# Kernel tuning notes

Measured on AMD Instinct MI355X. Metric: run time of the kernel, lower is better.

The kernel has to match this reference:

```python
import jax, jax.numpy as jnp
import numpy as np

B, S, D = 1, 4096, 1024
H, KVH, HD = 16, 4, 64  # heads, kv heads, head_dim; GQA groups = H//KVH
EOS_PROB = 0.05


def rotate_half(x):
    h = x.shape[-1] // 2
    return jnp.concatenate([-x[..., h:], x[..., :h]], axis=-1)


def setup_inputs() -> dict:
    key = jax.random.key(0)
    ks = jax.random.split(key, 8)
    hidden_states = jax.random.normal(ks[0], (B, S, D), jnp.float32) * 0.02
    # standard RoPE tables, [B, S, HD]
    inv_freq = 1.0 / (10000.0 ** (jnp.arange(0, HD, 2, dtype=jnp.float32) / HD))
    freqs = jnp.outer(jnp.arange(S, dtype=jnp.float32), inv_freq)
    emb = jnp.concatenate([freqs, freqs], axis=-1)
    cos = jnp.broadcast_to(jnp.cos(emb)[None], (B, S, HD))
    sin = jnp.broadcast_to(jnp.sin(emb)[None], (B, S, HD))
    sc = D ** -0.5
    Wq = jax.random.normal(ks[1], (D, H * HD), jnp.float32) * sc
    Wk = jax.random.normal(ks[2], (D, KVH * HD), jnp.float32) * sc
    Wv = jax.random.normal(ks[3], (D, KVH * HD), jnp.float32) * sc
    Wo = jax.random.normal(ks[4], (H * HD, D), jnp.float32) * sc
    # sentence-boundary (end-of-sentence / special) token mask, ~1 EOS per 20 tokens
    special = (jax.random.uniform(ks[5], (B, S)) < EOS_PROB).astype(jnp.int32)
    special = special.at[:, 0].set(1)  # BOS acts as a boundary token
    # closest end-of-sentence token index at or before each position
    pos = jnp.arange(S, dtype=jnp.int32)
    marked = jnp.where(special.astype(bool), pos[None, :], jnp.int32(-1))
    eos_idx = jax.lax.associative_scan(jnp.maximum, marked, axis=1)
    eos_idx = jnp.maximum(eos_idx, 0).astype(jnp.int32)
    return {
        'hidden_states': hidden_states, 'cos': cos, 'sin': sin,
        'Wq': Wq, 'Wk': Wk, 'Wv': Wv, 'Wo': Wo,
        'special_embeddings_mask': special,
        'clothest_end_of_sentence_token_idx': eos_idx,
    }


def reference(hidden_states, cos, sin, Wq, Wk, Wv, Wo,
              special_embeddings_mask, clothest_end_of_sentence_token_idx):
    b, s, d = hidden_states.shape
    # projections -> [b, h, s, hd]
    q = (hidden_states @ Wq).reshape(b, s, H, HD).transpose(0, 2, 1, 3)
    k = (hidden_states @ Wk).reshape(b, s, KVH, HD).transpose(0, 2, 1, 3)
    v = (hidden_states @ Wv).reshape(b, s, KVH, HD).transpose(0, 2, 1, 3)
    # RoPE
    c = cos[:, None, :, :]
    sn = sin[:, None, :, :]
    q = q * c + rotate_half(q) * sn
    k = k * c + rotate_half(k) * sn
    # GQA: repeat kv heads
    groups = H // KVH
    k = jnp.repeat(k, groups, axis=1)
    v = jnp.repeat(v, groups, axis=1)
    scores = jnp.einsum('bhqd,bhkd->bhqk', q, k) * (HD ** -0.5)
    # sentence-structured mask: causal AND (key inside current sentence OR key is
    # an end-of-sentence/special boundary token)
    pos = jnp.arange(s, dtype=jnp.int32)
    causal = (pos[None, :] <= pos[:, None])[None, None]           # [1,1,s,s]
    special_k = special_embeddings_mask.astype(bool)[:, None, None, :]  # [b,1,1,s]
    eos = clothest_end_of_sentence_token_idx[:, None, :, None]    # [b,1,s,1]
    allowed = causal & ((pos[None, None, None, :] >= eos) | special_k)
    scores = jnp.where(allowed, scores, jnp.asarray(-1e9, scores.dtype))
    probs = jax.nn.softmax(scores, axis=-1)
    attn = jnp.einsum('bhqk,bhkd->bhqd', probs, v)
    attn = attn.transpose(0, 2, 1, 3).reshape(b, s, H * HD)
    return attn @ Wo
```

## Files before the change

kernel.cpp:

```cpp
#include <hip/hip_runtime.h>

typedef __bf16 bf16x8 __attribute__((ext_vector_type(8)));
typedef float f32x4 __attribute__((ext_vector_type(4)));
typedef short s16x8 __attribute__((ext_vector_type(8)));
typedef short s16x4 __attribute__((ext_vector_type(4)));
typedef unsigned short u16;
typedef unsigned int u32;
typedef unsigned long long u64;

#define S_LEN 4096
#define DMODEL 1024
#define NH 16
#define HD 64

static __device__ __forceinline__ u16 f2bf(float f) {
  union { float f; u32 u; } a; a.f = f;
  u32 r = (a.u + 0x7fffu + ((a.u >> 16) & 1u)) >> 16;
  return (u16)r;
}

static __device__ __forceinline__ f32x4 mfma16(bf16x8 a, bf16x8 b, f32x4 c) {
  return __builtin_amdgcn_mfma_f32_16x16x32_bf16(a, b, c, 0, 0, 0);
}

static __device__ __forceinline__ f32x4 mfma16x16(s16x4 a, s16x4 b, f32x4 c) {
#if __has_builtin(__builtin_amdgcn_mfma_f32_16x16x16bf16_1k)
  return __builtin_amdgcn_mfma_f32_16x16x16bf16_1k(a, b, c, 0, 0, 0);
#else
  asm("v_mfma_f32_16x16x16_bf16 %0, %1, %2, %0" : "+v"(c) : "v"(a), "v"(b));
  return c;
#endif
}

static __device__ __forceinline__ void gload16(const void* g, void* l) {
  __builtin_amdgcn_global_load_lds((const __attribute__((address_space(1))) u32*)g,
                                   (__attribute__((address_space(3))) u32*)l, 16, 0, 0);
}

#define WAIT_VM(N) asm volatile("s_waitcnt vmcnt(" #N ")" ::: "memory")
static __device__ __forceinline__ void sbar() { __builtin_amdgcn_s_barrier(); }
static __device__ __forceinline__ void spin() { __builtin_amdgcn_sched_barrier(0); }

static __device__ __forceinline__ int xcd_swz(int id, int nwg) {
  return (id & 7) * (nwg >> 3) + (id >> 3);
}

__global__ __launch_bounds__(256)
void prep_kernel(const float* __restrict__ hidden, const float* __restrict__ Wq,
                 const float* __restrict__ Wk, const float* __restrict__ Wv,
                 const float* __restrict__ Wo, const int* __restrict__ spec,
                 const int* __restrict__ eosi,
                 u16* __restrict__ hbf, u16* __restrict__ wqkvT, u16* __restrict__ woT,
                 u64* __restrict__ spb, int* __restrict__ srank, int4* __restrict__ qmeta) {
  __shared__ float ftile[32][33];
  __shared__ u64 smask[64];
  __shared__ int scnt_s[64];
  __shared__ int spref[64];

  const int bx = (int)blockIdx.x;
  const int t = (int)threadIdx.x;

  if (bx < 4096) {
    const int i = (bx * 256 + t) * 4;
    const float4 v = *(const float4*)(hidden + i);
    uint2 o;
    o.x = (u32)f2bf(v.x) | ((u32)f2bf(v.y) << 16);
    o.y = (u32)f2bf(v.z) | ((u32)f2bf(v.w) << 16);
    *(uint2*)(hbf + i) = o;
    return;
  }
  if (bx < 6656) {
    const float* W; u16* WT; int N, loc, nbx;
    if (bx < 5120)      { W = Wq; WT = wqkvT;               N = 1024; loc = bx - 4096; nbx = 32; }
    else if (bx < 5376) { W = Wk; WT = wqkvT + 1024 * 1024; N = 256;  loc = bx - 5120; nbx = 8; }
    else if (bx < 5632) { W = Wv; WT = wqkvT + 1280 * 1024; N = 256;  loc = bx - 5376; nbx = 8; }
    else                { W = Wo; WT = woT;                 N = 1024; loc = bx - 5632; nbx = 32; }
    const int n0 = (loc % nbx) * 32, k0 = (loc / nbx) * 32;
    const int tx = t & 31, ty = t >> 5;
#pragma unroll
    for (int i = 0; i < 4; ++i)
      ftile[ty + 8 * i][tx] = W[(size_t)(k0 + ty + 8 * i) * N + n0 + tx];
    __syncthreads();
#pragma unroll
    for (int i = 0; i < 4; ++i)
      WT[(size_t)(n0 + ty + 8 * i) * 1024 + k0 + tx] = f2bf(ftile[tx][ty + 8 * i]);
    return;
  }
  const int wv = t >> 6, l = t & 63;
#pragma unroll
  for (int i = 0; i < 16; ++i) {
    const int b = wv * 16 + i;
    const u64 m = __ballot(spec[b * 64 + l] != 0);
    if (l == 0) { smask[b] = m; scnt_s[b] = __popcll(m); }
  }
  __syncthreads();
  if (wv == 0) {
    const int v = scnt_s[l];
    int inc = v;
#pragma unroll
    for (int d = 1; d < 64; d <<= 1) {
      const int o = __shfl_up(inc, d);
      if (l >= d) inc += o;
    }
    spref[l] = inc - v;
    spb[l] = smask[l];
  }
  __syncthreads();
#pragma unroll
  for (int i = 0; i < 16; ++i) {
    const int b = wv * 16 + i;
    const u64 m = smask[b];
    srank[b * 64 + l] = ((m >> l) & 1ull)
        ? spref[b] + __popcll(m & ((1ull << l) - 1ull)) : -1;
  }
  if (t < 64) {
    const int e = eosi[t * 64];
    const int tlo = e >> 6;
    const int nsp = spref[tlo];
    const int nspt = (nsp + 63) >> 6;
    qmeta[t] = make_int4(tlo, nspt, nspt + (t - tlo + 1), nsp);
  }
}

template <int MODE>
__global__ __launch_bounds__(256, 3)
void gemm128(const u16* __restrict__ A, const u16* __restrict__ BT,
             const float* __restrict__ cosp, const float* __restrict__ sinp,
             const int* __restrict__ srank,
             u16* __restrict__ Qb, u16* __restrict__ Kb, u16* __restrict__ Vtg,
             u16* __restrict__ Kg, u16* __restrict__ Vgt,
             float* __restrict__ Cf) {
  __shared__ __align__(16) u16 As[2][128 * 64];
  __shared__ __align__(16) u16 Bs[2][64 * 64];
  const int t = (int)threadIdx.x;
  const int w = t >> 6;
  const int lane = t & 63;
  const int lr = lane & 15, lg = lane >> 4;

  const int nx = (int)gridDim.x;
  const int nwg = nx * (int)gridDim.y;
  const int id = xcd_swz((int)blockIdx.x + (int)blockIdx.y * nx, nwg);
  const int m0 = (id / nx) * 128;
  const int n0 = (id % nx) * 64;
  const int wm = w * 32;

  f32x4 acc[2][4] = {};

  const int srow = t >> 3;
  const int sp = t & 7;

  auto STAGE = [&](int buf, int k0) {
#pragma unroll
    for (int i = 0; i < 4; ++i) {
      const int j = i * 32 + srow;
      gload16(A + (size_t)(m0 + j) * 1024 + k0 + ((sp ^ (j & 7)) * 8),
              &As[buf][i * 2048 + t * 8]);
    }
#pragma unroll
    for (int i = 0; i < 2; ++i) {
      const int j = i * 32 + srow;
      gload16(BT + (size_t)(n0 + j) * 1024 + k0 + ((sp ^ (j & 7)) * 8),
              &Bs[buf][i * 2048 + t * 8]);
    }
  };

  STAGE(0, 0);

  for (int it = 0; it < 16; ++it) {
    const int cur = it & 1;
    if (it < 15) {
      STAGE(cur ^ 1, (it + 1) * 64);
      WAIT_VM(6);
    } else {
      WAIT_VM(0);
    }
    spin();
    sbar();
#pragma unroll
    for (int c = 0; c < 2; ++c) {
      bf16x8 af[2], bg[4];
#pragma unroll
      for (int mi = 0; mi < 2; ++mi) {
        const int row = wm + mi * 16 + lr;
        af[mi] = *(const bf16x8*)&As[cur][row * 64 + (((c * 4 + lg) ^ (row & 7)) * 8)];
      }
#pragma unroll
      for (int ni = 0; ni < 4; ++ni) {
        const int row = ni * 16 + lr;
        bg[ni] = *(const bf16x8*)&Bs[cur][row * 64 + (((c * 4 + lg) ^ (row & 7)) * 8)];
      }
#pragma unroll
      for (int mi = 0; mi < 2; ++mi)
#pragma unroll
        for (int ni = 0; ni < 4; ++ni)
          acc[mi][ni] = mfma16(af[mi], bg[ni], acc[mi][ni]);
    }
    spin();
    sbar();
  }

  if (MODE == 0) {
#pragma unroll
    for (int mi = 0; mi < 2; ++mi)
#pragma unroll
      for (int r = 0; r < 4; ++r) {
        const int m = m0 + wm + mi * 16 + lg * 4 + r;
#pragma unroll
        for (int ni = 0; ni < 4; ++ni)
          Cf[(size_t)m * 1024 + n0 + ni * 16 + lr] = acc[mi][ni][r];
      }
  } else if (n0 < 1280) {
#pragma unroll
    for (int mi = 0; mi < 2; ++mi)
#pragma unroll
      for (int r = 0; r < 4; ++r) {
        const int m = m0 + wm + mi * 16 + lg * 4 + r;
        const float* cr = cosp + (size_t)m * 64;
        const float* sr = sinp + (size_t)m * 64;
        float o[4];
#pragma unroll
        for (int ni = 0; ni < 2; ++ni) {
          const int d1 = ni * 16 + lr, d2 = d1 + 32;
          const float x = acc[mi][ni][r], y = acc[mi][ni + 2][r];
          o[ni]     = x * cr[d1] - y * sr[d1];
          o[ni + 2] = y * cr[d2] + x * sr[d2];
        }
        if (n0 < 1024) {
          u16* dst = Qb + (size_t)m * 1024 + n0;
#pragma unroll
          for (int ni = 0; ni < 4; ++ni) dst[ni * 16 + lr] = f2bf(o[ni]);
        } else {
          u16 hv[4];
#pragma unroll
          for (int ni = 0; ni < 4; ++ni) hv[ni] = f2bf(o[ni]);
          u16* dst = Kb + (size_t)m * 256 + (n0 - 1024);
          const int sw = (m & 7) << 3;
#pragma unroll
          for (int ni = 0; ni < 4; ++ni) dst[(ni * 16 + lr) ^ sw] = hv[ni];
          const int rk = srank[m];
          if (rk >= 0) {
            u16* dg = Kg + (size_t)rk * 256 + (n0 - 1024);
            const int swg = (rk & 7) << 3;
#pragma unroll
            for (int ni = 0; ni < 4; ++ni) dg[(ni * 16 + lr) ^ swg] = hv[ni];
          }
        }
      }
  } else {
    const int kvh = (n0 - 1280) >> 6;
    int rks[2][4];
#pragma unroll
    for (int mi = 0; mi < 2; ++mi)
#pragma unroll
      for (int r = 0; r < 4; ++r)
        rks[mi][r] = srank[m0 + wm + mi * 16 + lg * 4 + r];
#pragma unroll
    for (int ni = 0; ni < 4; ++ni) {
      const int d = ni * 16 + lr;
      u16* vrow = Vtg + (size_t)(kvh * 64 + d) * 4096;
      u16* grow_ = Vgt + (size_t)(kvh * 64 + d) * 4096;
      const int xd = (d & 7) << 3;
#pragma unroll
      for (int mi = 0; mi < 2; ++mi) {
        const int sb = m0 + wm + mi * 16 + lg * 4;
        const int os = (sb & ~63) | ((sb & 63) ^ xd);
        u16 bv[4];
#pragma unroll
        for (int r = 0; r < 4; ++r) bv[r] = f2bf(acc[mi][ni][r]);
        uint2 pkv;
        pkv.x = (u32)bv[0] | ((u32)bv[1] << 16);
        pkv.y = (u32)bv[2] | ((u32)bv[3] << 16);
        *(uint2*)(vrow + os) = pkv;
#pragma unroll
        for (int r = 0; r < 4; ++r) {
          const int j = rks[mi][r];
          if (j >= 0) grow_[(j & ~63) + ((j & 63) ^ xd)] = bv[r];
        }
      }
    }
  }
}

__global__ __launch_bounds__(256, 5)
void attn_kernel(const u16* __restrict__ Qb, const u16* __restrict__ Kb,
                 const u16* __restrict__ Vtg, const u16* __restrict__ Kg,
                 const u16* __restrict__ Vgt, const u64* __restrict__ spb,
                 const int* __restrict__ eosi, const int4* __restrict__ qmeta,
                 u16* __restrict__ Ob) {
  __shared__ __align__(16) u16 lds[2][2][4096];

  const int id = xcd_swz((int)blockIdx.x + (int)blockIdx.y * 64, 1024);
  const int qt = 63 - (id & 63);
  const int h = id >> 6;
  const int kvh = h >> 2;
  const int t = (int)threadIdx.x;
  const int w = t >> 6;
  const int lane = t & 63;
  const int lr = lane & 15, lg = lane >> 4;
  const int q0 = qt * 64;
  const int q = q0 + w * 16 + lr;
  const int swl = (lr & 7) << 3;

  const int4 qm = qmeta[qt];
  const int tile_lo = qm.x;
  const int nit = qm.z;
  const int nsp = qm.w;
  const int nloc = qt - tile_lo + 1;

  bf16x8 aq[2];
  {
    const u16* qp = Qb + (size_t)q * 1024 + h * 64 + lg * 8;
    aq[0] = *(const bf16x8*)qp;
    aq[1] = *(const bf16x8*)(qp + 32);
  }
  const int eos_q = eosi[q];

  f32x4 acc[4] = {};
  float mrow = -3.0e38f;
  float lrow = 0.0f;

  const int grow = t >> 3;
  const int gcol = (t & 7) * 8;

  auto STAGE = [&](int buf, int it) {
    const u16 *kp, *vp;
    if (it < nloc) {
      const int kbase = (tile_lo + it) * 64;
      kp = Kb + (size_t)kbase * 256 + kvh * 64;
      vp = Vtg + (size_t)(kvh * 64) * 4096 + kbase;
    } else {
      const int jb = (it - nloc) * 64;
      kp = Kg + (size_t)jb * 256 + kvh * 64;
      vp = Vgt + (size_t)(kvh * 64) * 4096 + jb;
    }
#pragma unroll
    for (int i = 0; i < 2; ++i) {
      gload16(kp + (size_t)(i * 32 + grow) * 256 + gcol, &lds[buf][0][i * 2048 + t * 8]);
      gload16(vp + (size_t)(i * 32 + grow) * 4096 + gcol, &lds[buf][1][i * 2048 + t * 8]);
    }
  };

  STAGE(0, 0);

  for (int it = 0; it < nit; ++it) {
    if (it + 1 < nit) {
      STAGE((it + 1) & 1, it + 1);
      WAIT_VM(4);
    } else {
      WAIT_VM(0);
    }
    spin();
    sbar();
    const u16* Kl = &lds[it & 1][0][0];
    const u16* Vl = &lds[it & 1][1][0];

    f32x4 st[4];
#pragma unroll
    for (int kt = 0; kt < 4; ++kt) {
      f32x4 s = {};
#pragma unroll
      for (int c = 0; c < 2; ++c) {
        bf16x8 ak = *(const bf16x8*)(Kl + (kt * 16 + lr) * 64 + ((c * 32 + lg * 8) ^ swl));
        s = mfma16(ak, aq[c], s);
      }
      st[kt] = s;
    }

    u64 allowed;
    if (it < nloc) {
      const int kbase = (tile_lo + it) * 64;
      const u64 spec = spb[tile_lo + it];
      const int dq = q - kbase;
      const u64 causal = (dq >= 63) ? ~0ull : ((2ull << dq) - 1ull);
      const int de = eos_q - kbase;
      const u64 ge = (de <= 0) ? ~0ull : (de >= 64 ? 0ull : (~0ull << de));
      allowed = causal & (ge | spec);
    } else {
      const int rem = nsp - (it - nloc) * 64;
      allowed = (rem >= 64) ? ~0ull : ((1ull << rem) - 1ull);
    }

    float xs[16];
    float tmax = -3.0e38f;
#pragma unroll
    for (int kt = 0; kt < 4; ++kt) {
      const u32 bits = (u32)(allowed >> (kt * 16 + lg * 4)) & 0xFu;
#pragma unroll
      for (int r = 0; r < 4; ++r) {
        const float x = ((bits >> r) & 1u) ? st[kt][r] * 0.18033688011112042f : -3.0e38f;
        xs[kt * 4 + r] = x;
        tmax = fmaxf(tmax, x);
      }
    }
    tmax = fmaxf(tmax, __shfl_xor(tmax, 16));
    tmax = fmaxf(tmax, __shfl_xor(tmax, 32));
    const float mn = fmaxf(mrow, tmax);
    const float resc = exp2f(mrow - mn);
    mrow = mn;

    float rs = 0.0f;
    u32 pk[8];
#pragma unroll
    for (int i = 0; i < 16; i += 2) {
      const float p0 = exp2f(xs[i] - mn);
      const float p1 = exp2f(xs[i + 1] - mn);
      rs += p0 + p1;
      pk[i >> 1] = (u32)f2bf(p0) | ((u32)f2bf(p1) << 16);
    }
    rs += __shfl_xor(rs, 16);
    rs += __shfl_xor(rs, 32);
    lrow = lrow * resc + rs;

#pragma unroll
    for (int dt = 0; dt < 4; ++dt)
#pragma unroll
      for (int r = 0; r < 4; ++r) acc[dt][r] *= resc;

#pragma unroll
    for (int kt = 0; kt < 4; ++kt) {
      union { u32 u[2]; s16x4 v; } cv;
      cv.u[0] = pk[kt * 2]; cv.u[1] = pk[kt * 2 + 1];
      const int vo = (kt * 16 + lg * 4) ^ swl;
#pragma unroll
      for (int dt = 0; dt < 4; ++dt) {
        s16x4 av = *(const s16x4*)(Vl + (dt * 16 + lr) * 64 + vo);
        acc[dt] = mfma16x16(av, cv.v, acc[dt]);
      }
    }
    spin();
    sbar();
  }

  const float inv = 1.0f / lrow;
#pragma unroll
  for (int dt = 0; dt < 4; ++dt) {
    const u32 w0 = (u32)f2bf(acc[dt][0] * inv) | ((u32)f2bf(acc[dt][1] * inv) << 16);
    const u32 w1 = (u32)f2bf(acc[dt][2] * inv) | ((u32)f2bf(acc[dt][3] * inv) << 16);
    u32* dst = (u32*)(Ob + (size_t)q * 1024 + h * 64 + dt * 16 + lg * 4);
    dst[0] = w0; dst[1] = w1;
  }
}

extern "C" void kernel_launch(void* const* d_in, const int* in_sizes, int n_in,
                              void* d_out, int out_size, void* d_ws, size_t ws_size,
                              hipStream_t stream) {
  (void)in_sizes; (void)n_in; (void)out_size; (void)ws_size;
  const float* hidden = (const float*)d_in[0];
  const float* cosp   = (const float*)d_in[1];
  const float* sinp   = (const float*)d_in[2];
  const float* Wq     = (const float*)d_in[3];
  const float* Wk     = (const float*)d_in[4];
  const float* Wv     = (const float*)d_in[5];
  const float* Wo     = (const float*)d_in[6];
  const int* spec     = (const int*)d_in[7];
  const int* eosi     = (const int*)d_in[8];
  float* out = (float*)d_out;

  u16* ws = (u16*)d_ws;
  u16* hbf   = ws;
  u16* wqkvT = hbf + 4194304;
  u16* woT   = wqkvT + 1572864;
  u16* Qb    = woT + 1048576;
  u16* Kb    = Qb + 4194304;
  u16* Vtg   = Kb + 1048576;
  u16* Ob    = Vtg + 1048576;
  u16* tail  = Ob + 4194304;
  u64* spb   = (u64*)tail;
  int* srank = (int*)(tail + 256);
  int4* qmeta = (int4*)(tail + 8448);
  u16* Kg    = tail + 8960;
  u16* Vgt   = Kg + 1048576;

  prep_kernel<<<dim3(6657), dim3(256), 0, stream>>>(hidden, Wq, Wk, Wv, Wo, spec, eosi,
                                                    hbf, wqkvT, woT, spb, srank, qmeta);
  gemm128<1><<<dim3(24, 32), dim3(256), 0, stream>>>(hbf, wqkvT, cosp, sinp, srank,
                                                     Qb, Kb, Vtg, Kg, Vgt, nullptr);
  attn_kernel<<<dim3(64, 16), dim3(256), 0, stream>>>(Qb, Kb, Vtg, Kg, Vgt, spb,
                                                      eosi, qmeta, Ob);
  gemm128<0><<<dim3(16, 32), dim3(256), 0, stream>>>(Ob, woT, nullptr, nullptr, nullptr,
                                                     nullptr, nullptr, nullptr, nullptr,
                                                     nullptr, out);
}
```

Baseline: 75.30 us.

## Process two GQA query heads per attention block to share K/V tiles

Each attention block now handles two query heads that map to the same KV head. Every K/V tile it stages into LDS is reused for both heads' QK^T, softmax and PV work, which halves global and LDS staging traffic per unit of work. The cost is a grid of half as many blocks, more registers per thread (two sets of accumulators and Q fragments), and a lower occupancy hint in launch bounds. That can hurt latency hiding and load balance across CUs, given the causal work imbalance between query tiles.

```diff
diff --git a/kernel.cpp b/kernel.cpp
--- a/kernel.cpp
+++ b/kernel.cpp
@@ -281,7 +281,7 @@
   }
 }
 
-__global__ __launch_bounds__(256, 5)
+__global__ __launch_bounds__(256, 4)
 void attn_kernel(const u16* __restrict__ Qb, const u16* __restrict__ Kb,
                  const u16* __restrict__ Vtg, const u16* __restrict__ Kg,
                  const u16* __restrict__ Vgt, const u64* __restrict__ spb,
@@ -289,10 +289,11 @@
                  u16* __restrict__ Ob) {
   __shared__ __align__(16) u16 lds[2][2][4096];
 
-  const int id = xcd_swz((int)blockIdx.x + (int)blockIdx.y * 64, 1024);
+  const int id = xcd_swz((int)blockIdx.x + (int)blockIdx.y * 32, 512);
   const int qt = 63 - (id & 63);
-  const int h = id >> 6;
-  const int kvh = h >> 2;
+  const int hp = id >> 6;
+  const int h0 = hp * 2;
+  const int kvh = hp >> 1;
   const int t = (int)threadIdx.x;
   const int w = t >> 6;
   const int lane = t & 63;
@@ -307,17 +308,18 @@
   const int nsp = qm.w;
   const int nloc = qt - tile_lo + 1;
 
-  bf16x8 aq[2];
-  {
-    const u16* qp = Qb + (size_t)q * 1024 + h * 64 + lg * 8;
-    aq[0] = *(const bf16x8*)qp;
-    aq[1] = *(const bf16x8*)(qp + 32);
+  bf16x8 aq[2][2];
+#pragma unroll
+  for (int hd = 0; hd < 2; ++hd) {
+    const u16* qp = Qb + (size_t)q * 1024 + (h0 + hd) * 64 + lg * 8;
+    aq[hd][0] = *(const bf16x8*)qp;
+    aq[hd][1] = *(const bf16x8*)(qp + 32);
   }
   const int eos_q = eosi[q];
 
-  f32x4 acc[4] = {};
-  float mrow = -3.0e38f;
-  float lrow = 0.0f;
+  f32x4 acc[2][4] = {};
+  float mrow[2] = {-3.0e38f, -3.0e38f};
+  float lrow[2] = {0.0f, 0.0f};
 
   const int grow = t >> 3;
   const int gcol = (t & 7) * 8;
@@ -353,18 +355,6 @@
     sbar();
     const u16* Kl = &lds[it & 1][0][0];
     const u16* Vl = &lds[it & 1][1][0];
-
-    f32x4 st[4];
-#pragma unroll
-    for (int kt = 0; kt < 4; ++kt) {
-      f32x4 s = {};
-#pragma unroll
-      for (int c = 0; c < 2; ++c) {
-        bf16x8 ak = *(const bf16x8*)(Kl + (kt * 16 + lr) * 64 + ((c * 32 + lg * 8) ^ swl));
-        s = mfma16(ak, aq[c], s);
-      }
-      st[kt] = s;
-    }
 
     u64 allowed;
     if (it < nloc) {
@@ -380,64 +370,82 @@
       allowed = (rem >= 64) ? ~0ull : ((1ull << rem) - 1ull);
     }
 
-    float xs[16];
-    float tmax = -3.0e38f;
-#pragma unroll
-    for (int kt = 0; kt < 4; ++kt) {
-      const u32 bits = (u32)(allowed >> (kt * 16 + lg * 4)) & 0xFu;
-#pragma unroll
-      for (int r = 0; r < 4; ++r) {
-        const float x = ((bits >> r) & 1u) ? st[kt][r] * 0.18033688011112042f : -3.0e38f;
-        xs[kt * 4 + r] = x;
-        tmax = fmaxf(tmax, x);
-      }
-    }
-    tmax = fmaxf(tmax, __shfl_xor(tmax, 16));
-    tmax = fmaxf(tmax, __shfl_xor(tmax, 32));
-    const float mn = fmaxf(mrow, tmax);
-    const float resc = exp2f(mrow - mn);
-    mrow = mn;
-
-    float rs = 0.0f;
-    u32 pk[8];
-#pragma unroll
-    for (int i = 0; i < 16; i += 2) {
-      const float p0 = exp2f(xs[i] - mn);
-      const float p1 = exp2f(xs[i + 1] - mn);
-      rs += p0 + p1;
-      pk[i >> 1] = (u32)f2bf(p0) | ((u32)f2bf(p1) << 16);
-    }
-    rs += __shfl_xor(rs, 16);
-    rs += __shfl_xor(rs, 32);
-    lrow = lrow * resc + rs;
-
-#pragma unroll
-    for (int dt = 0; dt < 4; ++dt)
-#pragma unroll
-      for (int r = 0; r < 4; ++r) acc[dt][r] *= resc;
-
-#pragma unroll
-    for (int kt = 0; kt < 4; ++kt) {
-      union { u32 u[2]; s16x4 v; } cv;
-      cv.u[0] = pk[kt * 2]; cv.u[1] = pk[kt * 2 + 1];
-      const int vo = (kt * 16 + lg * 4) ^ swl;
-#pragma unroll
-      for (int dt = 0; dt < 4; ++dt) {
-        s16x4 av = *(const s16x4*)(Vl + (dt * 16 + lr) * 64 + vo);
-        acc[dt] = mfma16x16(av, cv.v, acc[dt]);
+#pragma unroll
+    for (int hd = 0; hd < 2; ++hd) {
+      f32x4 st[4];
+#pragma unroll
+      for (int kt = 0; kt < 4; ++kt) {
+        f32x4 s = {};
+#pragma unroll
+        for (int c = 0; c < 2; ++c) {
+          bf16x8 ak = *(const bf16x8*)(Kl + (kt * 16 + lr) * 64 + ((c * 32 + lg * 8) ^ swl));
+          s = mfma16(ak, aq[hd][c], s);
+        }
+        st[kt] = s;
+      }
+
+      float xs[16];
+      float tmax = -3.0e38f;
+#pragma unroll
+      for (int kt = 0; kt < 4; ++kt) {
+        const u32 bits = (u32)(allowed >> (kt * 16 + lg * 4)) & 0xFu;
+#pragma unroll
+        for (int r = 0; r < 4; ++r) {
+          const float x = ((bits >> r) & 1u) ? st[kt][r] * 0.18033688011112042f : -3.0e38f;
+          xs[kt * 4 + r] = x;
+          tmax = fmaxf(tmax, x);
+        }
+      }
+      tmax = fmaxf(tmax, __shfl_xor(tmax, 16));
+      tmax = fmaxf(tmax, __shfl_xor(tmax, 32));
+      const float mn = fmaxf(mrow[hd], tmax);
+      const float resc = exp2f(mrow[hd] - mn);
+      mrow[hd] = mn;
+
+      float rs = 0.0f;
+      u32 pk[8];
+#pragma unroll
+      for (int i = 0; i < 16; i += 2) {
+        const float p0 = exp2f(xs[i] - mn);
+        const float p1 = exp2f(xs[i + 1] - mn);
+        rs += p0 + p1;
+        pk[i >> 1] = (u32)f2bf(p0) | ((u32)f2bf(p1) << 16);
+      }
+      rs += __shfl_xor(rs, 16);
+      rs += __shfl_xor(rs, 32);
+      lrow[hd] = lrow[hd] * resc + rs;
+
+#pragma unroll
+      for (int dt = 0; dt < 4; ++dt)
+#pragma unroll
+        for (int r = 0; r < 4; ++r) acc[hd][dt][r] *= resc;
+
+#pragma unroll
+      for (int kt = 0; kt < 4; ++kt) {
+        union { u32 u[2]; s16x4 v; } cv;
+        cv.u[0] = pk[kt * 2]; cv.u[1] = pk[kt * 2 + 1];
+        const int vo = (kt * 16 + lg * 4) ^ swl;
+#pragma unroll
+        for (int dt = 0; dt < 4; ++dt) {
+          s16x4 av = *(const s16x4*)(Vl + (dt * 16 + lr) * 64 + vo);
+          acc[hd][dt] = mfma16x16(av, cv.v, acc[hd][dt]);
+        }
       }
     }
     spin();
     sbar();
   }
 
-  const float inv = 1.0f / lrow;
-#pragma unroll
-  for (int dt = 0; dt < 4; ++dt) {
-    const u32 w0 = (u32)f2bf(acc[dt][0] * inv) | ((u32)f2bf(acc[dt][1] * inv) << 16);
-    const u32 w1 = (u32)f2bf(acc[dt][2] * inv) | ((u32)f2bf(acc[dt][3] * inv) << 16);
-    u32* dst = (u32*)(Ob + (size_t)q * 1024 + h * 64 + dt * 16 + lg * 4);
-    dst[0] = w0; dst[1] = w1;
+#pragma unroll
+  for (int hd = 0; hd < 2; ++hd) {
+    const float inv = 1.0f / lrow[hd];
+#pragma unroll
+    for (int dt = 0; dt < 4; ++dt) {
+      const u32 w0 = (u32)f2bf(acc[hd][dt][0] * inv) | ((u32)f2bf(acc[hd][dt][1] * inv) << 16);
+      const u32 w1 = (u32)f2bf(acc[hd][dt][2] * inv) | ((u32)f2bf(acc[hd][dt][3] * inv) << 16);
+      u32* dst = (u32*)(Ob + (size_t)q * 1024 + (h0 + hd) * 64 + dt * 16 + lg * 4);
+      dst[0] = w0; dst[1] = w1;
+    }
   }
 }
 
@@ -475,7 +483,7 @@
                                                     hbf, wqkvT, woT, spb, srank, qmeta);
   gemm128<1><<<dim3(24, 32), dim3(256), 0, stream>>>(hbf, wqkvT, cosp, sinp, srank,
                                                      Qb, Kb, Vtg, Kg, Vgt, nullptr);
-  attn_kernel<<<dim3(64, 16), dim3(256), 0, stream>>>(Qb, Kb, Vtg, Kg, Vgt, spb,
+  attn_kernel<<<dim3(32, 16), dim3(256), 0, stream>>>(Qb, Kb, Vtg, Kg, Vgt, spb,
                                                       eosi, qmeta, Ob);
   gemm128<0><<<dim3(16, 32), dim3(256), 0, stream>>>(Ob, woT, nullptr, nullptr, nullptr,
                                                      nullptr, nullptr, nullptr, nullptr,
```

New measurement: 78.36 us. 1.04x slower.
